# Optimization experiments

Measured on AMD Instinct MI355X. Metric: run time of the kernel, lower is better.

Reference implementation:

```python
import jax, jax.numpy as jnp
import numpy as np

N, E, F, H, C = 50000, 800000, 64, 64, 10


def setup_inputs() -> dict:
    key = jax.random.key(0)
    ks = jax.random.split(key, 9)
    x = jax.random.normal(ks[0], (N, F), dtype=jnp.float32)
    edge_index = jax.random.randint(ks[1], (2, E), 0, N, dtype=jnp.int64)
    s_f = 1.0 / np.sqrt(F)
    s_h = 1.0 / np.sqrt(H)
    return {
        "x": x,
        "edge_index": edge_index,
        # ChebConv(F->H, K=1): only Theta_0
        "W1_0": jax.random.normal(ks[2], (F, H), dtype=jnp.float32) * s_f,
        "b1": jnp.zeros((H,), dtype=jnp.float32),
        # ChebConv(H->H, K=2): Theta_0, Theta_1
        "W2_0": jax.random.normal(ks[3], (H, H), dtype=jnp.float32) * s_h,
        "W2_1": jax.random.normal(ks[4], (H, H), dtype=jnp.float32) * s_h,
        "b2": jnp.zeros((H,), dtype=jnp.float32),
        # final Linear(H->C)
        "Wl": jax.random.normal(ks[5], (H, C), dtype=jnp.float32) * s_h,
        "bl": jnp.zeros((C,), dtype=jnp.float32),
    }


def reference(x, edge_index, W1_0, b1, W2_0, W2_1, b2, Wl, bl):
    n = x.shape[0]
    src, dst = edge_index[0], edge_index[1]
    # Scaled Laplacian (PyG ChebConv, sym norm, lambda_max=2.0):
    # L_hat = -D^{-1/2} A D^{-1/2}  (self-loop terms cancel: +1 scaled, then -1 added)
    deg = jax.ops.segment_sum(jnp.ones((src.shape[0],), dtype=x.dtype), src,
                              num_segments=n)
    dis = jnp.where(deg > 0, jax.lax.rsqrt(jnp.maximum(deg, 1.0)), 0.0)
    w = -(dis[src] * dis[dst])  # [E]

    def lap(h):  # L_hat @ h via edge-wise gather/scatter
        return jax.ops.segment_sum(w[:, None] * h[src], dst, num_segments=n)

    # conv1 (K=1): T0 = x only -> plain linear
    h = jax.nn.relu(x @ W1_0 + b1)
    # dropout is identity in eval mode
    x_res = h
    # conv2 (K=2): T0 = h, T1 = L_hat h
    h2 = jax.nn.relu(h @ W2_0 + lap(h) @ W2_1 + b2)
    out = (h2 + x_res) @ Wl + bl
    return jax.nn.log_softmax(out, axis=1)
```

## Files before the change

kernel.cpp:

```cpp
#include <hip/hip_runtime.h>
#include <math.h>
#include <stdint.h>


#define NBKT 256
#define BCAP 5120
#define CHUNK 2048
#define RB 12800
#define NSLICE 64

__device__ __forceinline__ unsigned short f2bf(float f) {
    uint32_t u; __builtin_memcpy(&u, &f, 4);
    u += 0x7fffu + ((u >> 16) & 1u);
    return (unsigned short)(u >> 16);
}
__device__ __forceinline__ float bf2f(unsigned short s) {
    uint32_t u = (uint32_t)s << 16; float f; __builtin_memcpy(&f, &u, 4);
    return f;
}
__device__ __forceinline__ float lo_of(uint32_t u) {
    uint32_t v = u << 16; float f; __builtin_memcpy(&f, &v, 4); return f;
}
__device__ __forceinline__ float hi_of(uint32_t u) {
    uint32_t v = u & 0xffff0000u; float f; __builtin_memcpy(&f, &v, 4); return f;
}

__global__ __launch_bounds__(256) void binA_kernel(const int* __restrict__ ei,
                                                   int* __restrict__ gcur,
                                                   uint32_t* __restrict__ pairs,
                                                   int E) {
    __shared__ uint32_t stage[CHUNK];
    __shared__ int cnt[NBKT], obase[NBKT], goff[NBKT], curs[NBKT];
    __shared__ int wpart[4], stot;
    int t = threadIdx.x, lane = t & 63, wv = t >> 6;
    int e0 = blockIdx.x * CHUNK;
    int s[8], d[8];
    bool val[8];
#pragma unroll
    for (int j = 0; j < 8; ++j) {
        int e = e0 + j * 256 + t;
        val[j] = e < E;
        s[j] = val[j] ? ei[e] : 0;
        d[j] = val[j] ? ei[E + e] : 0;
    }
    cnt[t] = 0;
    __syncthreads();
#pragma unroll
    for (int j = 0; j < 8; ++j)
        if (val[j]) atomicAdd(&cnt[d[j] >> 8], 1);
    __syncthreads();
    int cv = cnt[t];
    int v = cv;
#pragma unroll
    for (int dd = 1; dd < 64; dd <<= 1) {
        int u = __shfl_up(v, dd);
        if (lane >= dd) v += u;
    }
    if (lane == 63) wpart[wv] = v;
    __syncthreads();
    if (t == 0) {
        int r = 0;
#pragma unroll
        for (int w = 0; w < 4; ++w) { int tmp = wpart[w]; wpart[w] = r; r += tmp; }
        stot = r;
    }
    __syncthreads();
    int eb = wpart[wv] + v - cv;
    obase[t] = eb;
    curs[t] = eb;
    goff[t] = (cv > 0) ? atomicAdd(&gcur[t], cv) : 0;
    __syncthreads();
#pragma unroll
    for (int j = 0; j < 8; ++j)
        if (val[j]) {
            int b = d[j] >> 8;
            int pos = atomicAdd(&curs[b], 1);
            stage[pos] = ((uint32_t)d[j] << 16) | (uint32_t)s[j];
        }
    __syncthreads();
    int tot = stot;
    for (int k = t; k < tot; k += 256) {
        uint32_t u = stage[k];
        int b = (int)(u >> 24);
        int slot = goff[b] + (k - obase[b]);
        if (slot < BCAP) pairs[(size_t)b * BCAP + slot] = u;
    }
}

__global__ __launch_bounds__(256) void deghist_kernel(const int* __restrict__ ei,
                                                      int* __restrict__ degS,
                                                      int E, int n) {
    __shared__ int bins[RB];
    int t = threadIdx.x;
    int r = blockIdx.x & 3;
    int sl = blockIdx.x >> 2;
    int lo = r * RB;
    for (int i = t; i < RB; i += 256) bins[i] = 0;
    __syncthreads();
    int per = (E + NSLICE - 1) / NSLICE;
    int b0 = sl * per, b1 = b0 + per; if (b1 > E) b1 = E;
    for (int e = b0 + t; e < b1; e += 256) {
        int s = ei[e] - lo;
        if ((unsigned)s < (unsigned)RB) atomicAdd(&bins[s], 1);
    }
    __syncthreads();
    int hi = n - lo; if (hi > RB) hi = RB;
    for (int i = t; i < hi; i += 256) {
        int v = bins[i];
        if (v) atomicAdd(&degS[lo + i], v);
    }
}

__global__ __launch_bounds__(256) void binB_kernel(const int* __restrict__ gcur,
                                                   const uint32_t* __restrict__ pairs,
                                                   int* __restrict__ csr,
                                                   int* __restrict__ rowptr,
                                                   int* __restrict__ cntD,
                                                   const int* __restrict__ degS,
                                                   float* __restrict__ dis, int n) {
    __shared__ int hist[NBKT], obase[NBKT], curs[NBKT];
    __shared__ int wpart[4];
    int t = threadIdx.x, lane = t & 63, wv = t >> 6;
    int b = blockIdx.x;
    {
        int node = b * 256 + t;
        if (node < n) {
            int dsum = degS[node];
            dis[node] = (dsum > 0) ? rsqrtf((float)dsum) : 0.0f;
        }
    }
    int nb = gcur[b]; if (nb > BCAP) nb = BCAP;
    hist[t] = 0;
    __syncthreads();
    const uint32_t* bp = pairs + (size_t)b * BCAP;
    for (int k = t; k < nb; k += 256) {
        int ld = (int)((bp[k] >> 16) & 255);
        atomicAdd(&hist[ld], 1);
    }
    __syncthreads();
    int cv = hist[t];
    int v = cv;
#pragma unroll
    for (int dd = 1; dd < 64; dd <<= 1) {
        int u = __shfl_up(v, dd);
        if (lane >= dd) v += u;
    }
    if (lane == 63) wpart[wv] = v;
    __syncthreads();
    if (t == 0) {
        int r = 0;
#pragma unroll
        for (int w = 0; w < 4; ++w) { int tmp = wpart[w]; wpart[w] = r; r += tmp; }
    }
    __syncthreads();
    int eb = wpart[wv] + v - cv;
    obase[t] = eb;
    curs[t] = eb;
    int node = b * 256 + t;
    if (node < n) {
        rowptr[node] = b * BCAP + eb;
        cntD[node] = cv;
    }
    __syncthreads();
    for (int k = t; k < nb; k += 256) {
        uint32_t u = bp[k];
        int ld = (int)((u >> 16) & 255);
        int pos = atomicAdd(&curs[ld], 1);
        csr[(size_t)b * BCAP + pos] = (int)(u & 0xffffu);
    }
}

__global__ __launch_bounds__(256) void gemm3_kernel(const float* __restrict__ x,
                                                    const float* __restrict__ W1,
                                                    const float* __restrict__ b1,
                                                    const float* __restrict__ W20,
                                                    const float* __restrict__ W21,
                                                    const float* __restrict__ b2,
                                                    const float* __restrict__ dis,
                                                    unsigned short* __restrict__ h16,
                                                    unsigned short* __restrict__ p16,
                                                    unsigned short* __restrict__ g16,
                                                    int n) {
    __shared__ __align__(16) float sA[64][68];
    __shared__ __align__(16) float sW1[64][64];
    __shared__ __align__(16) float sW20[64][64];
    __shared__ __align__(16) float sW21[64][64];
    int t = threadIdx.x;
    for (int i = t; i < 4096; i += 256) {
        sW1[i >> 6][i & 63] = W1[i];
        sW20[i >> 6][i & 63] = W20[i];
        sW21[i >> 6][i & 63] = W21[i];
    }
    int r0 = blockIdx.x * 64;
    {
        int rr0 = t >> 4, k0 = (t & 15) * 4;
        for (int rr = rr0; rr < 64; rr += 16) {
            int grow = r0 + rr;
            float4 v = make_float4(0.f, 0.f, 0.f, 0.f);
            if (grow < n) v = *(const float4*)&x[(size_t)grow * 64 + k0];
            sA[k0][rr] = v.x; sA[k0 + 1][rr] = v.y;
            sA[k0 + 2][rr] = v.z; sA[k0 + 3][rr] = v.w;
        }
    }
    __syncthreads();
    int tr = t >> 4, tc = t & 15;

    float acc[4][4] = {};
    for (int k = 0; k < 64; ++k) {
        float4 a = *(const float4*)&sA[k][tr * 4];
        float4 b = *(const float4*)&sW1[k][tc * 4];
        float av[4] = {a.x, a.y, a.z, a.w};
        float bv[4] = {b.x, b.y, b.z, b.w};
#pragma unroll
        for (int i = 0; i < 4; ++i)
#pragma unroll
            for (int j = 0; j < 4; ++j) acc[i][j] = fmaf(av[i], bv[j], acc[i][j]);
    }
    float4 bv1 = *(const float4*)&b1[tc * 4];
    float hv[4][4];
#pragma unroll
    for (int i = 0; i < 4; ++i) {
        hv[i][0] = fmaxf(acc[i][0] + bv1.x, 0.f);
        hv[i][1] = fmaxf(acc[i][1] + bv1.y, 0.f);
        hv[i][2] = fmaxf(acc[i][2] + bv1.z, 0.f);
        hv[i][3] = fmaxf(acc[i][3] + bv1.w, 0.f);
    }
#pragma unroll
    for (int i = 0; i < 4; ++i) {
        int grow = r0 + tr * 4 + i;
        if (grow < n) {
            ushort4 o;
            o.x = f2bf(hv[i][0]); o.y = f2bf(hv[i][1]);
            o.z = f2bf(hv[i][2]); o.w = f2bf(hv[i][3]);
            *(ushort4*)&h16[(size_t)grow * 64 + tc * 4] = o;
        }
    }
    __syncthreads();
#pragma unroll
    for (int i = 0; i < 4; ++i)
#pragma unroll
        for (int j = 0; j < 4; ++j) sA[tc * 4 + j][tr * 4 + i] = hv[i][j];
    __syncthreads();

    float accP[4][4] = {}, accG[4][4] = {};
    for (int k = 0; k < 64; ++k) {
        float4 a = *(const float4*)&sA[k][tr * 4];
        float4 bp = *(const float4*)&sW20[k][tc * 4];
        float4 bg = *(const float4*)&sW21[k][tc * 4];
        float av[4] = {a.x, a.y, a.z, a.w};
        float bpv[4] = {bp.x, bp.y, bp.z, bp.w};
        float bgv[4] = {bg.x, bg.y, bg.z, bg.w};
#pragma unroll
        for (int i = 0; i < 4; ++i)
#pragma unroll
            for (int j = 0; j < 4; ++j) {
                accP[i][j] = fmaf(av[i], bpv[j], accP[i][j]);
                accG[i][j] = fmaf(av[i], bgv[j], accG[i][j]);
            }
    }
    float4 bv2 = *(const float4*)&b2[tc * 4];
#pragma unroll
    for (int i = 0; i < 4; ++i) {
        int grow = r0 + tr * 4 + i;
        if (grow < n) {
            float dr = dis[grow];
            ushort4 op, og;
            op.x = f2bf(accP[i][0] + bv2.x); op.y = f2bf(accP[i][1] + bv2.y);
            op.z = f2bf(accP[i][2] + bv2.z); op.w = f2bf(accP[i][3] + bv2.w);
            og.x = f2bf(dr * accG[i][0]); og.y = f2bf(dr * accG[i][1]);
            og.z = f2bf(dr * accG[i][2]); og.w = f2bf(dr * accG[i][3]);
            *(ushort4*)&p16[(size_t)grow * 64 + tc * 4] = op;
            *(ushort4*)&g16[(size_t)grow * 64 + tc * 4] = og;
        }
    }
}

__global__ __launch_bounds__(256, 8) void gather_out_kernel(
        const int* __restrict__ rowptr, const int* __restrict__ cntD,
        const int* __restrict__ csr, const float* __restrict__ dis,
        const uint32_t* __restrict__ gp, const uint32_t* __restrict__ pp,
        const uint32_t* __restrict__ hp, const float* __restrict__ Wl,
        const float* __restrict__ bl, float* __restrict__ out, int n) {
    __shared__ __align__(16) float so[4][68];
    __shared__ __align__(16) float sWlT[10][68];
    __shared__ float sout[4][12];
    int t = threadIdx.x;
    if (t < 160) {
        float4 w = *(const float4*)&Wl[t * 4];
        int i0 = t * 4;
        sWlT[i0 % 10][i0 / 10] = w.x;
        sWlT[(i0 + 1) % 10][(i0 + 1) / 10] = w.y;
        sWlT[(i0 + 2) % 10][(i0 + 2) / 10] = w.z;
        sWlT[(i0 + 3) % 10][(i0 + 3) / 10] = w.w;
    }
    int p = t & 31;
    int eslot = (t >> 5) & 1;
    int wid = __builtin_amdgcn_readfirstlane(t >> 6);
    int row = blockIdx.x * 4 + wid;
    if (row < n) {
        int m = cntD[row], rs = rowptr[row];
        float disd = dis[row];
        float l0 = 0.f, l1 = 0.f, l2 = 0.f, l3 = 0.f;
        float h0 = 0.f, h1 = 0.f, h2a = 0.f, h3 = 0.f;
        int k = 0;
        for (; k + 16 <= m; k += 16) {
            int sA0 = csr[rs + k + 0],  sA1 = csr[rs + k + 1];
            int sA2 = csr[rs + k + 2],  sA3 = csr[rs + k + 3];
            int sA4 = csr[rs + k + 4],  sA5 = csr[rs + k + 5];
            int sA6 = csr[rs + k + 6],  sA7 = csr[rs + k + 7];
            int sA8 = csr[rs + k + 8],  sA9 = csr[rs + k + 9];
            int sAa = csr[rs + k + 10], sAb = csr[rs + k + 11];
            int sAc = csr[rs + k + 12], sAd = csr[rs + k + 13];
            int sAe = csr[rs + k + 14], sAf = csr[rs + k + 15];
            int e0 = eslot ? sA1 : sA0;
            int e1 = eslot ? sA3 : sA2;
            int e2 = eslot ? sA5 : sA4;
            int e3 = eslot ? sA7 : sA6;
            int e4 = eslot ? sA9 : sA8;
            int e5 = eslot ? sAb : sAa;
            int e6 = eslot ? sAd : sAc;
            int e7 = eslot ? sAf : sAe;
            uint32_t u0 = gp[(size_t)e0 * 32 + p];
            uint32_t u1 = gp[(size_t)e1 * 32 + p];
            uint32_t u2 = gp[(size_t)e2 * 32 + p];
            uint32_t u3 = gp[(size_t)e3 * 32 + p];
            uint32_t u4 = gp[(size_t)e4 * 32 + p];
            uint32_t u5 = gp[(size_t)e5 * 32 + p];
            uint32_t u6 = gp[(size_t)e6 * 32 + p];
            uint32_t u7 = gp[(size_t)e7 * 32 + p];
            l0 += lo_of(u0); h0 += hi_of(u0);
            l1 += lo_of(u1); h1 += hi_of(u1);
            l2 += lo_of(u2); h2a += hi_of(u2);
            l3 += lo_of(u3); h3 += hi_of(u3);
            l0 += lo_of(u4); h0 += hi_of(u4);
            l1 += lo_of(u5); h1 += hi_of(u5);
            l2 += lo_of(u6); h2a += hi_of(u6);
            l3 += lo_of(u7); h3 += hi_of(u7);
        }
        for (; k + 2 <= m; k += 2) {
            int s0 = csr[rs + k], s1 = csr[rs + k + 1];
            int e = eslot ? s1 : s0;
            uint32_t u = gp[(size_t)e * 32 + p];
            l0 += lo_of(u); h0 += hi_of(u);
        }
        if (k < m) {
            int s0 = csr[rs + k];
            if (eslot == 0) {
                uint32_t u = gp[(size_t)s0 * 32 + p];
                l0 += lo_of(u); h0 += hi_of(u);
            }
        }
        float alo = (l0 + l1) + (l2 + l3);
        float ahi = (h0 + h1) + (h2a + h3);
        alo += __shfl_xor(alo, 32);
        ahi += __shfl_xor(ahi, 32);
        uint32_t up = pp[(size_t)row * 32 + p];
        uint32_t uh = hp[(size_t)row * 32 + p];
        float h2lo = fmaxf(lo_of(up) - disd * alo, 0.f) + lo_of(uh);
        float h2hi = fmaxf(hi_of(up) - disd * ahi, 0.f) + hi_of(uh);
        if (eslot == 0) {
            so[wid][2 * p] = h2lo;
            so[wid][2 * p + 1] = h2hi;
        }
    }
    __syncthreads();
    if (t < 40) {
        int r = t / 10, j = t % 10;
        float acc = bl[j];
#pragma unroll
        for (int k0 = 0; k0 < 64; k0 += 4) {
            float4 a = *(const float4*)&so[r][k0];
            float4 b = *(const float4*)&sWlT[j][k0];
            acc = fmaf(a.x, b.x, acc);
            acc = fmaf(a.y, b.y, acc);
            acc = fmaf(a.z, b.z, acc);
            acc = fmaf(a.w, b.w, acc);
        }
        sout[r][j] = acc;
    }
    __syncthreads();
    if (t < 64) {
        int r = t >> 4, l16 = t & 15;
        float v = (l16 < 10) ? sout[r][l16] : -1e30f;
        float mm = v;
#pragma unroll
        for (int d = 1; d < 16; d <<= 1) mm = fmaxf(mm, __shfl_xor(mm, d, 16));
        float e = (l16 < 10) ? expf(v - mm) : 0.f;
        float ss = e;
#pragma unroll
        for (int d = 1; d < 16; d <<= 1) ss += __shfl_xor(ss, d, 16);
        int grow = blockIdx.x * 4 + r;
        if (grow < n && l16 < 10)
            out[(size_t)grow * 10 + l16] = v - mm - logf(ss);
    }
}

extern "C" void kernel_launch(void* const* d_in, const int* in_sizes, int n_in,
                              void* d_out, int out_size, void* d_ws, size_t ws_size,
                              hipStream_t stream) {
    const float* x   = (const float*)d_in[0];
    const int*   ei  = (const int*)d_in[1];
    const float* W1  = (const float*)d_in[2];
    const float* b1  = (const float*)d_in[3];
    const float* W20 = (const float*)d_in[4];
    const float* W21 = (const float*)d_in[5];
    const float* b2  = (const float*)d_in[6];
    const float* Wl  = (const float*)d_in[7];
    const float* bl  = (const float*)d_in[8];
    float* out = (float*)d_out;

    int n = in_sizes[0] / 64;
    int E = in_sizes[1] / 2;

    char* ws = (char*)d_ws;
    size_t off = 0;
    auto alloc = [&](size_t bytes) {
        void* p = ws + off;
        off = (off + bytes + 255) & ~(size_t)255;
        return p;
    };
    int*       gcur   = (int*)alloc((size_t)NBKT * 4);
    uint32_t*  pairs  = (uint32_t*)alloc((size_t)NBKT * BCAP * 4);
    int*       csr    = (int*)alloc((size_t)NBKT * BCAP * 4);
    int*       rowptr = (int*)alloc((size_t)n * 4);
    int*       cntD   = (int*)alloc((size_t)n * 4);
    int*       degS   = (int*)alloc((size_t)n * 4);
    float*     dis    = (float*)alloc((size_t)n * 4);
    unsigned short* h16 = (unsigned short*)alloc((size_t)n * 64 * 2);
    unsigned short* p16 = (unsigned short*)alloc((size_t)n * 64 * 2);
    unsigned short* g16 = (unsigned short*)alloc((size_t)n * 64 * 2);

    hipMemsetAsync(gcur, 0, (size_t)NBKT * 4, stream);
    hipMemsetAsync(degS, 0, (size_t)n * 4, stream);

    int nchunk = (E + CHUNK - 1) / CHUNK;
    binA_kernel<<<nchunk, 256, 0, stream>>>(ei, gcur, pairs, E);
    deghist_kernel<<<4 * NSLICE, 256, 0, stream>>>(ei, degS, E, n);
    binB_kernel<<<NBKT, 256, 0, stream>>>(gcur, pairs, csr, rowptr, cntD, degS, dis, n);
    gemm3_kernel<<<(n + 63) / 64, 256, 0, stream>>>(x, W1, b1, W20, W21, b2, dis,
                                                    h16, p16, g16, n);
    gather_out_kernel<<<(n + 3) / 4, 256, 0, stream>>>(rowptr, cntD, csr, dis,
                                                       (const uint32_t*)g16,
                                                       (const uint32_t*)p16,
                                                       (const uint32_t*)h16,
                                                       Wl, bl, out, n);
}
```

Measured before the change: 187.6 us.

## Use bf16 MFMA with swizzled LDS for the fused dense GEMM kernel

Replaces the scalar FP32 FMA tiling in the fused x@W1 / h@W20 / h@W21 kernel with 16x16x32 bf16 MFMA instructions. Inputs and weights are converted to bf16 into XOR-swizzled shared memory to avoid bank conflicts, and W20/W21 are concatenated into one 128-column transposed tile. The first GEMM now runs in bf16 instead of fp32, which adds precision loss. Output stores become scalar 2-byte writes, which may be less coalesced than the previous ushort4 stores.

```diff
diff --git a/kernel.cpp b/kernel.cpp
--- a/kernel.cpp
+++ b/kernel.cpp
@@ -8,6 +8,9 @@
 #define CHUNK 2048
 #define RB 12800
 #define NSLICE 64
+
+typedef __attribute__((ext_vector_type(8))) short bf16x8;
+typedef __attribute__((ext_vector_type(4))) float f32x4;
 
 __device__ __forceinline__ unsigned short f2bf(float f) {
     uint32_t u; __builtin_memcpy(&u, &f, 4);
@@ -181,96 +184,109 @@
                                                     unsigned short* __restrict__ p16,
                                                     unsigned short* __restrict__ g16,
                                                     int n) {
-    __shared__ __align__(16) float sA[64][68];
-    __shared__ __align__(16) float sW1[64][64];
-    __shared__ __align__(16) float sW20[64][64];
-    __shared__ __align__(16) float sW21[64][64];
+    __shared__ __align__(16) unsigned short sA[64 * 64];
+    __shared__ __align__(16) unsigned short sW1T[64 * 64];
+    __shared__ __align__(16) unsigned short sW2T[128 * 64];
+    __shared__ float sDis[64], sB1[64], sB2[64];
     int t = threadIdx.x;
-    for (int i = t; i < 4096; i += 256) {
-        sW1[i >> 6][i & 63] = W1[i];
-        sW20[i >> 6][i & 63] = W20[i];
-        sW21[i >> 6][i & 63] = W21[i];
-    }
     int r0 = blockIdx.x * 64;
+    if (t < 64) {
+        sB1[t] = b1[t];
+        sB2[t] = b2[t];
+        int grow = r0 + t;
+        sDis[t] = (grow < n) ? dis[grow] : 0.f;
+    }
+    for (int idx = t; idx < 4096; idx += 256) {
+        int k = idx >> 6, o = idx & 63;
+        int byte = (o * 128 + k * 2) ^ ((o & 7) << 4);
+        *(unsigned short*)((char*)sW1T + byte) = f2bf(W1[idx]);
+        *(unsigned short*)((char*)sW2T + byte) = f2bf(W20[idx]);
+        int byte2 = ((o + 64) * 128 + k * 2) ^ ((o & 7) << 4);
+        *(unsigned short*)((char*)sW2T + byte2) = f2bf(W21[idx]);
+    }
     {
-        int rr0 = t >> 4, k0 = (t & 15) * 4;
-        for (int rr = rr0; rr < 64; rr += 16) {
-            int grow = r0 + rr;
+        int rr = t >> 4, k0 = (t & 15) * 4;
+        for (int r = rr; r < 64; r += 16) {
+            int grow = r0 + r;
             float4 v = make_float4(0.f, 0.f, 0.f, 0.f);
             if (grow < n) v = *(const float4*)&x[(size_t)grow * 64 + k0];
-            sA[k0][rr] = v.x; sA[k0 + 1][rr] = v.y;
-            sA[k0 + 2][rr] = v.z; sA[k0 + 3][rr] = v.w;
-        }
-    }
-    __syncthreads();
-    int tr = t >> 4, tc = t & 15;
-
-    float acc[4][4] = {};
-    for (int k = 0; k < 64; ++k) {
-        float4 a = *(const float4*)&sA[k][tr * 4];
-        float4 b = *(const float4*)&sW1[k][tc * 4];
-        float av[4] = {a.x, a.y, a.z, a.w};
-        float bv[4] = {b.x, b.y, b.z, b.w};
-#pragma unroll
-        for (int i = 0; i < 4; ++i)
-#pragma unroll
-            for (int j = 0; j < 4; ++j) acc[i][j] = fmaf(av[i], bv[j], acc[i][j]);
-    }
-    float4 bv1 = *(const float4*)&b1[tc * 4];
-    float hv[4][4];
-#pragma unroll
-    for (int i = 0; i < 4; ++i) {
-        hv[i][0] = fmaxf(acc[i][0] + bv1.x, 0.f);
-        hv[i][1] = fmaxf(acc[i][1] + bv1.y, 0.f);
-        hv[i][2] = fmaxf(acc[i][2] + bv1.z, 0.f);
-        hv[i][3] = fmaxf(acc[i][3] + bv1.w, 0.f);
-    }
-#pragma unroll
-    for (int i = 0; i < 4; ++i) {
-        int grow = r0 + tr * 4 + i;
-        if (grow < n) {
-            ushort4 o;
-            o.x = f2bf(hv[i][0]); o.y = f2bf(hv[i][1]);
-            o.z = f2bf(hv[i][2]); o.w = f2bf(hv[i][3]);
-            *(ushort4*)&h16[(size_t)grow * 64 + tc * 4] = o;
-        }
-    }
-    __syncthreads();
-#pragma unroll
-    for (int i = 0; i < 4; ++i)
-#pragma unroll
-        for (int j = 0; j < 4; ++j) sA[tc * 4 + j][tr * 4 + i] = hv[i][j];
-    __syncthreads();
-
-    float accP[4][4] = {}, accG[4][4] = {};
-    for (int k = 0; k < 64; ++k) {
-        float4 a = *(const float4*)&sA[k][tr * 4];
-        float4 bp = *(const float4*)&sW20[k][tc * 4];
-        float4 bg = *(const float4*)&sW21[k][tc * 4];
-        float av[4] = {a.x, a.y, a.z, a.w};
-        float bpv[4] = {bp.x, bp.y, bp.z, bp.w};
-        float bgv[4] = {bg.x, bg.y, bg.z, bg.w};
-#pragma unroll
-        for (int i = 0; i < 4; ++i)
-#pragma unroll
-            for (int j = 0; j < 4; ++j) {
-                accP[i][j] = fmaf(av[i], bpv[j], accP[i][j]);
-                accG[i][j] = fmaf(av[i], bgv[j], accG[i][j]);
+            ushort4 u;
+            u.x = f2bf(v.x); u.y = f2bf(v.y); u.z = f2bf(v.z); u.w = f2bf(v.w);
+            int byte = (r * 128 + k0 * 2) ^ ((r & 7) << 4);
+            *(ushort4*)((char*)sA + byte) = u;
+        }
+    }
+    __syncthreads();
+    int w = t >> 6, l = t & 63;
+    int lr = l & 15, kg = l >> 4;
+
+    bf16x8 a0, a1;
+    {
+        int row = 16 * w + lr;
+        int sw = (row & 7) << 4;
+        a0 = *(bf16x8*)((char*)sA + ((row * 128 + kg * 16) ^ sw));
+        a1 = *(bf16x8*)((char*)sA + ((row * 128 + 64 + kg * 16) ^ sw));
+    }
+    float hreg[4][4];
+#pragma unroll
+    for (int ct = 0; ct < 4; ++ct) {
+        int orow = ct * 16 + lr;
+        int sw = (orow & 7) << 4;
+        bf16x8 bb0 = *(bf16x8*)((char*)sW1T + ((orow * 128 + kg * 16) ^ sw));
+        bf16x8 bb1 = *(bf16x8*)((char*)sW1T + ((orow * 128 + 64 + kg * 16) ^ sw));
+        f32x4 acc = {0.f, 0.f, 0.f, 0.f};
+        acc = __builtin_amdgcn_mfma_f32_16x16x32_bf16(a0, bb0, acc, 0, 0, 0);
+        acc = __builtin_amdgcn_mfma_f32_16x16x32_bf16(a1, bb1, acc, 0, 0, 0);
+        float bias = sB1[ct * 16 + lr];
+#pragma unroll
+        for (int j = 0; j < 4; ++j) hreg[ct][j] = fmaxf(acc[j] + bias, 0.f);
+    }
+#pragma unroll
+    for (int ct = 0; ct < 4; ++ct)
+#pragma unroll
+        for (int j = 0; j < 4; ++j) {
+            int grow = r0 + 16 * w + kg * 4 + j;
+            if (grow < n) h16[(size_t)grow * 64 + ct * 16 + lr] = f2bf(hreg[ct][j]);
+        }
+    __syncthreads();
+#pragma unroll
+    for (int ct = 0; ct < 4; ++ct)
+#pragma unroll
+        for (int j = 0; j < 4; ++j) {
+            int row = 16 * w + kg * 4 + j;
+            int col = ct * 16 + lr;
+            int byte = (row * 128 + col * 2) ^ ((row & 7) << 4);
+            *(unsigned short*)((char*)sA + byte) = f2bf(hreg[ct][j]);
+        }
+    __syncthreads();
+
+    {
+        int row = 16 * w + lr;
+        int sw = (row & 7) << 4;
+        a0 = *(bf16x8*)((char*)sA + ((row * 128 + kg * 16) ^ sw));
+        a1 = *(bf16x8*)((char*)sA + ((row * 128 + 64 + kg * 16) ^ sw));
+    }
+#pragma unroll
+    for (int ct = 0; ct < 8; ++ct) {
+        int orow = ct * 16 + lr;
+        int sw = (orow & 7) << 4;
+        bf16x8 bb0 = *(bf16x8*)((char*)sW2T + ((orow * 128 + kg * 16) ^ sw));
+        bf16x8 bb1 = *(bf16x8*)((char*)sW2T + ((orow * 128 + 64 + kg * 16) ^ sw));
+        f32x4 acc = {0.f, 0.f, 0.f, 0.f};
+        acc = __builtin_amdgcn_mfma_f32_16x16x32_bf16(a0, bb0, acc, 0, 0, 0);
+        acc = __builtin_amdgcn_mfma_f32_16x16x32_bf16(a1, bb1, acc, 0, 0, 0);
+#pragma unroll
+        for (int j = 0; j < 4; ++j) {
+            int row = 16 * w + kg * 4 + j;
+            int grow = r0 + row;
+            if (grow >= n) continue;
+            if (ct < 4) {
+                int col = ct * 16 + lr;
+                p16[(size_t)grow * 64 + col] = f2bf(acc[j] + sB2[col]);
+            } else {
+                int col = (ct - 4) * 16 + lr;
+                g16[(size_t)grow * 64 + col] = f2bf(sDis[row] * acc[j]);
             }
-    }
-    float4 bv2 = *(const float4*)&b2[tc * 4];
-#pragma unroll
-    for (int i = 0; i < 4; ++i) {
-        int grow = r0 + tr * 4 + i;
-        if (grow < n) {
-            float dr = dis[grow];
-            ushort4 op, og;
-            op.x = f2bf(accP[i][0] + bv2.x); op.y = f2bf(accP[i][1] + bv2.y);
-            op.z = f2bf(accP[i][2] + bv2.z); op.w = f2bf(accP[i][3] + bv2.w);
-            og.x = f2bf(dr * accG[i][0]); og.y = f2bf(dr * accG[i][1]);
-            og.z = f2bf(dr * accG[i][2]); og.w = f2bf(dr * accG[i][3]);
-            *(ushort4*)&p16[(size_t)grow * 64 + tc * 4] = op;
-            *(ushort4*)&g16[(size_t)grow * 64 + tc * 4] = og;
         }
     }
 }
```

Result: faster. 175.9 us (-6.2%).
